# Optimization experiments

Hardware: AMD Instinct MI355X
Metric: run time of the kernel (lower is better)

Reference implementation:

```python
import jax, jax.numpy as jnp
import numpy as np

EMBED = 64
ATT_FACTOR = 10
N_FIELDS = 50
BATCH = 2048


def setup_inputs() -> dict:
    key = jax.random.key(0)
    k_x, k_w, k_h, k_p = jax.random.split(key, 4)
    x = jax.random.normal(k_x, (BATCH, N_FIELDS, EMBED), dtype=jnp.float32)
    # xavier-normal-ish init for params
    attention_W = jax.random.normal(k_w, (EMBED, ATT_FACTOR), dtype=jnp.float32) * (2.0 / (EMBED + ATT_FACTOR)) ** 0.5
    attention_b = jnp.zeros((ATT_FACTOR,), dtype=jnp.float32)
    projection_h = jax.random.normal(k_h, (ATT_FACTOR, 1), dtype=jnp.float32) * (2.0 / (ATT_FACTOR + 1)) ** 0.5
    projection_p = jax.random.normal(k_p, (EMBED, 1), dtype=jnp.float32) * (2.0 / (EMBED + 1)) ** 0.5
    return {"x": x, "attention_W": attention_W, "attention_b": attention_b,
            "projection_h": projection_h, "projection_p": projection_p}


def reference(x, attention_W, attention_b, projection_h, projection_p):
    F_ = x.shape[1]
    idx_i, idx_j = np.triu_indices(F_, k=1)  # all pairs (i<j), P = F*(F-1)/2
    inter = x[:, idx_i, :] * x[:, idx_j, :]  # [B, P, E]
    att_tmp = jax.nn.relu(jnp.einsum('bpe,ef->bpf', inter, attention_W) + attention_b)  # [B,P,A]
    logits = jnp.einsum('bpf,fo->bpo', att_tmp, projection_h)  # [B,P,1]
    score = jax.nn.softmax(logits, axis=1)  # softmax over pairs
    att_out = jnp.sum(score * inter, axis=1)  # [B, E]
    # dropout is identity at inference
    return att_out @ projection_p  # [B, 1]
```

## Files before the change

kernel.cpp:

```cpp
#include <hip/hip_runtime.h>
#include <math.h>


#define F_ 50
#define E_ 64
#define A_ 10
#define XSTR 72
#define NT 256
#define LOG2E 1.44269504088896f

typedef _Float16 half8 __attribute__((ext_vector_type(8)));
typedef _Float16 half4t __attribute__((ext_vector_type(4)));
typedef float f32x4 __attribute__((ext_vector_type(4)));

__global__ __launch_bounds__(NT, 2)
void afm_kernel(const float* __restrict__ x,
                const float* __restrict__ W,
                const float* __restrict__ bias,
                const float* __restrict__ h,
                const float* __restrict__ pp,
                float* __restrict__ out, int nbatch) {
  __shared__ __align__(16) _Float16 sXh[4 * 64 * XSTR];
  __shared__ __align__(16) _Float16 sWh[(A_ + 1) * E_];
  __shared__ float sb[A_], sh[A_];

  const int tid = threadIdx.x;
  const int lane = tid & 63, w4 = tid >> 6;
  const int b = blockIdx.x * 4 + w4;
  const bool bvalid = b < nbatch;
  _Float16* xb = sXh + w4 * (64 * XSTR);

  if (bvalid) {
    const float4* xs = (const float4*)(x + (size_t)b * (F_ * E_));
    for (int q = lane; q < F_ * 16; q += 64) {
      float4 v = xs[q];
      int f = q >> 4, e4 = q & 15;
      half4t hv = {(_Float16)v.x, (_Float16)v.y, (_Float16)v.z, (_Float16)v.w};
      *(half4t*)(xb + f * XSTR + e4 * 4) = hv;
    }
  }
  for (int q = lane; q < 14 * 8; q += 64) {
    int f = F_ + (q >> 3), c = q & 7;
    half8 z = {};
    *(half8*)(xb + f * XSTR + c * 8) = z;
  }
  if (tid < 11 * 16) {
    int k = tid >> 4, e4 = tid & 15;
    float v0, v1, v2, v3;
    if (k < A_) {
      v0 = W[(e4 * 4 + 0) * A_ + k]; v1 = W[(e4 * 4 + 1) * A_ + k];
      v2 = W[(e4 * 4 + 2) * A_ + k]; v3 = W[(e4 * 4 + 3) * A_ + k];
    } else {
      float4 t4 = *(const float4*)(pp + e4 * 4);
      v0 = t4.x; v1 = t4.y; v2 = t4.z; v3 = t4.w;
    }
    half4t hv = {(_Float16)v0, (_Float16)v1, (_Float16)v2, (_Float16)v3};
    *(half4t*)(sWh + k * E_ + e4 * 4) = hv;
  }
  if (tid < A_) { sb[tid] = bias[tid]; sh[tid] = h[tid] * LOG2E; }
  __syncthreads();

  float num = 0.f, den = 0.f;
  if (bvalid) {
    const int m = lane & 15, q8 = lane >> 4;
    half8 fr[4][2];
#pragma unroll
    for (int bi = 0; bi < 4; ++bi)
#pragma unroll
      for (int es = 0; es < 2; ++es)
        fr[bi][es] = *(const half8*)(xb + (bi * 16 + m) * XSTR + es * 32 + q8 * 8);

    float lg[10][4];
#pragma unroll
    for (int t0 = 0; t0 < 10; ++t0)
#pragma unroll
      for (int r = 0; r < 4; ++r) lg[t0][r] = 0.f;

#pragma unroll 1
    for (int k = 0; k < A_; ++k) {
      half8 wv0 = *(const half8*)(sWh + k * E_ + q8 * 8);
      half8 wv1 = *(const half8*)(sWh + k * E_ + 32 + q8 * 8);
      float bk = sb[k];
      f32x4 ci = {bk, bk, bk, bk};
      half8 sa0[4];
#pragma unroll
      for (int bi = 0; bi < 4; ++bi) sa0[bi] = fr[bi][0] * wv0;
      f32x4 t[10];
      {
        int idx = 0;
#pragma unroll
        for (int bi = 0; bi < 4; ++bi)
#pragma unroll
          for (int bj = bi; bj < 4; ++bj)
            t[idx++] = __builtin_amdgcn_mfma_f32_16x16x32_f16(sa0[bi], fr[bj][0], ci, 0, 0, 0);
      }
      half8 sa1[4];
#pragma unroll
      for (int bi = 0; bi < 4; ++bi) sa1[bi] = fr[bi][1] * wv1;
      {
        int idx = 0;
#pragma unroll
        for (int bi = 0; bi < 4; ++bi)
#pragma unroll
          for (int bj = bi; bj < 4; ++bj) {
            t[idx] = __builtin_amdgcn_mfma_f32_16x16x32_f16(sa1[bi], fr[bj][1], t[idx], 0, 0, 0);
            ++idx;
          }
      }
      float hk = sh[k];
#pragma unroll
      for (int idx = 0; idx < 10; ++idx)
#pragma unroll
        for (int r = 0; r < 4; ++r)
          lg[idx][r] = fmaf(fmaxf(t[idx][r], 0.f), hk, lg[idx][r]);
    }

    half8 pv0 = *(const half8*)(sWh + A_ * E_ + q8 * 8);
    half8 pv1 = *(const half8*)(sWh + A_ * E_ + 32 + q8 * 8);
    f32x4 z4 = {0.f, 0.f, 0.f, 0.f};
    int idx = 0;
#pragma unroll
    for (int bi = 0; bi < 4; ++bi) {
      half8 pa0 = fr[bi][0] * pv0;
      half8 pa1 = fr[bi][1] * pv1;
#pragma unroll
      for (int bj = bi; bj < 4; ++bj) {
        f32x4 s4 = __builtin_amdgcn_mfma_f32_16x16x32_f16(pa0, fr[bj][0], z4, 0, 0, 0);
        s4 = __builtin_amdgcn_mfma_f32_16x16x32_f16(pa1, fr[bj][1], s4, 0, 0, 0);
#pragma unroll
        for (int r = 0; r < 4; ++r) {
          int irow = bi * 16 + q8 * 4 + r;
          int jcol = bj * 16 + m;
          bool valid = (irow < jcol) && (jcol < F_);
          float w = valid ? exp2f(lg[idx][r]) : 0.f;
          num = fmaf(w, s4[r], num);
          den += w;
        }
        ++idx;
      }
    }
  }

#pragma unroll
  for (int off = 32; off; off >>= 1) {
    num += __shfl_down(num, off);
    den += __shfl_down(den, off);
  }
  if (lane == 0 && bvalid) out[b] = num / den;
}

extern "C" void kernel_launch(void* const* d_in, const int* in_sizes, int n_in,
                              void* d_out, int out_size, void* d_ws, size_t ws_size,
                              hipStream_t stream) {
  const float* x  = (const float*)d_in[0];
  const float* W  = (const float*)d_in[1];
  const float* bb = (const float*)d_in[2];
  const float* h  = (const float*)d_in[3];
  const float* pp = (const float*)d_in[4];
  float* out = (float*)d_out;
  const int nbatch = in_sizes[0] / (F_ * E_);
  const int nblocks = (nbatch + 3) / 4;
  afm_kernel<<<nblocks, NT, 0, stream>>>(x, W, bb, h, pp, out, nbatch);
}
```

Before: 87.92 us.

## Split each batch's pair-tile work across two wavefronts per sample

Each batch element is now handled by two wavefronts instead of one. The 10 upper-triangular 16x16 tiles are split 5/5 between them via compile-time tile tables, and the partial numerator and denominator are combined through shared memory. Launch bounds rise to 4 blocks per CU, and halving the shared x buffer and the per-thread logit registers is meant to raise occupancy and cut per-wave serial MFMA latency. In exchange, 128 threads cooperate on each x load, a block-wide barrier is added, and each wave loads fragments it may not fully use.

```diff
diff --git a/kernel.cpp b/kernel.cpp
--- a/kernel.cpp
+++ b/kernel.cpp
@@ -13,34 +13,116 @@
 typedef _Float16 half4t __attribute__((ext_vector_type(4)));
 typedef float f32x4 __attribute__((ext_vector_type(4)));
 
-__global__ __launch_bounds__(NT, 2)
+template <int PW>
+__device__ __forceinline__ void compute_half(const _Float16* __restrict__ xb,
+                                             const _Float16* __restrict__ sWh,
+                                             const float* __restrict__ sb,
+                                             const float* __restrict__ sh,
+                                             int lane, float& num, float& den) {
+  constexpr int TI[5] = { PW ? 1 : 0, PW ? 1 : 0, PW ? 2 : 0, PW ? 2 : 0, PW ? 3 : 1 };
+  constexpr int TJ[5] = { PW ? 2 : 0, PW ? 3 : 1, PW ? 2 : 2, PW ? 3 : 3, PW ? 3 : 1 };
+  constexpr bool NEED[4] = { PW == 0, true, PW != 0, PW != 0 };
+
+  const int m = lane & 15, q8 = lane >> 4;
+
+  half8 fr[4][2];
+#pragma unroll
+  for (int bi = 0; bi < 4; ++bi)
+#pragma unroll
+    for (int es = 0; es < 2; ++es)
+      fr[bi][es] = *(const half8*)(xb + (bi * 16 + m) * XSTR + es * 32 + q8 * 8);
+
+  float lg[5][4];
+#pragma unroll
+  for (int tt = 0; tt < 5; ++tt)
+#pragma unroll
+    for (int r = 0; r < 4; ++r) lg[tt][r] = 0.f;
+
+#pragma unroll 1
+  for (int k = 0; k < A_; ++k) {
+    half8 wv0 = *(const half8*)(sWh + k * E_ + q8 * 8);
+    half8 wv1 = *(const half8*)(sWh + k * E_ + 32 + q8 * 8);
+    float bk = sb[k];
+    f32x4 ci = { bk, bk, bk, bk };
+    half8 sa[4];
+#pragma unroll
+    for (int bi = 0; bi < 4; ++bi)
+      if constexpr (true) { if (NEED[bi]) sa[bi] = fr[bi][0] * wv0; }
+    f32x4 t[5];
+#pragma unroll
+    for (int tt = 0; tt < 5; ++tt)
+      t[tt] = __builtin_amdgcn_mfma_f32_16x16x32_f16(sa[TI[tt]], fr[TJ[tt]][0], ci, 0, 0, 0);
+#pragma unroll
+    for (int bi = 0; bi < 4; ++bi)
+      if (NEED[bi]) sa[bi] = fr[bi][1] * wv1;
+#pragma unroll
+    for (int tt = 0; tt < 5; ++tt)
+      t[tt] = __builtin_amdgcn_mfma_f32_16x16x32_f16(sa[TI[tt]], fr[TJ[tt]][1], t[tt], 0, 0, 0);
+    float hk = sh[k];
+#pragma unroll
+    for (int tt = 0; tt < 5; ++tt)
+#pragma unroll
+      for (int r = 0; r < 4; ++r)
+        lg[tt][r] = fmaf(fmaxf(t[tt][r], 0.f), hk, lg[tt][r]);
+  }
+
+  half8 pv0 = *(const half8*)(sWh + A_ * E_ + q8 * 8);
+  half8 pv1 = *(const half8*)(sWh + A_ * E_ + 32 + q8 * 8);
+  half8 pa0[4], pa1[4];
+#pragma unroll
+  for (int bi = 0; bi < 4; ++bi)
+    if (NEED[bi]) { pa0[bi] = fr[bi][0] * pv0; pa1[bi] = fr[bi][1] * pv1; }
+  f32x4 z4 = { 0.f, 0.f, 0.f, 0.f };
+#pragma unroll
+  for (int tt = 0; tt < 5; ++tt) {
+    f32x4 s4 = __builtin_amdgcn_mfma_f32_16x16x32_f16(pa0[TI[tt]], fr[TJ[tt]][0], z4, 0, 0, 0);
+    s4 = __builtin_amdgcn_mfma_f32_16x16x32_f16(pa1[TI[tt]], fr[TJ[tt]][1], s4, 0, 0, 0);
+#pragma unroll
+    for (int r = 0; r < 4; ++r) {
+      int irow = TI[tt] * 16 + q8 * 4 + r;
+      int jcol = TJ[tt] * 16 + m;
+      bool valid = (irow < jcol) && (jcol < F_);
+      float w = valid ? exp2f(lg[tt][r]) : 0.f;
+      num = fmaf(w, s4[r], num);
+      den += w;
+    }
+  }
+}
+
+__global__ __launch_bounds__(NT, 4)
 void afm_kernel(const float* __restrict__ x,
                 const float* __restrict__ W,
                 const float* __restrict__ bias,
                 const float* __restrict__ h,
                 const float* __restrict__ pp,
                 float* __restrict__ out, int nbatch) {
-  __shared__ __align__(16) _Float16 sXh[4 * 64 * XSTR];
+  __shared__ __align__(16) _Float16 sXh[2 * 64 * XSTR];
   __shared__ __align__(16) _Float16 sWh[(A_ + 1) * E_];
   __shared__ float sb[A_], sh[A_];
+  __shared__ float rn[4], rd[4];
 
   const int tid = threadIdx.x;
   const int lane = tid & 63, w4 = tid >> 6;
-  const int b = blockIdx.x * 4 + w4;
+  const int pair = tid >> 7, t128 = tid & 127;
+  const int b = blockIdx.x * 2 + pair;
   const bool bvalid = b < nbatch;
-  _Float16* xb = sXh + w4 * (64 * XSTR);
+  _Float16* xb = sXh + pair * (64 * XSTR);
 
   if (bvalid) {
     const float4* xs = (const float4*)(x + (size_t)b * (F_ * E_));
-    for (int q = lane; q < F_ * 16; q += 64) {
-      float4 v = xs[q];
-      int f = q >> 4, e4 = q & 15;
-      half4t hv = {(_Float16)v.x, (_Float16)v.y, (_Float16)v.z, (_Float16)v.w};
-      *(half4t*)(xb + f * XSTR + e4 * 4) = hv;
+#pragma unroll
+    for (int it = 0; it < 7; ++it) {
+      int q = t128 + it * 128;
+      if (it < 6 || q < F_ * 16) {
+        float4 v = xs[q];
+        int f = q >> 4, e4 = q & 15;
+        half4t hv = { (_Float16)v.x, (_Float16)v.y, (_Float16)v.z, (_Float16)v.w };
+        *(half4t*)(xb + f * XSTR + e4 * 4) = hv;
+      }
     }
   }
-  for (int q = lane; q < 14 * 8; q += 64) {
-    int f = F_ + (q >> 3), c = q & 7;
+  if (t128 < 112) {
+    int f = F_ + (t128 >> 3), c = t128 & 7;
     half8 z = {};
     *(half8*)(xb + f * XSTR + c * 8) = z;
   }
@@ -54,7 +136,7 @@
       float4 t4 = *(const float4*)(pp + e4 * 4);
       v0 = t4.x; v1 = t4.y; v2 = t4.z; v3 = t4.w;
     }
-    half4t hv = {(_Float16)v0, (_Float16)v1, (_Float16)v2, (_Float16)v3};
+    half4t hv = { (_Float16)v0, (_Float16)v1, (_Float16)v2, (_Float16)v3 };
     *(half4t*)(sWh + k * E_ + e4 * 4) = hv;
   }
   if (tid < A_) { sb[tid] = bias[tid]; sh[tid] = h[tid] * LOG2E; }
@@ -62,83 +144,8 @@
 
   float num = 0.f, den = 0.f;
   if (bvalid) {
-    const int m = lane & 15, q8 = lane >> 4;
-    half8 fr[4][2];
-#pragma unroll
-    for (int bi = 0; bi < 4; ++bi)
-#pragma unroll
-      for (int es = 0; es < 2; ++es)
-        fr[bi][es] = *(const half8*)(xb + (bi * 16 + m) * XSTR + es * 32 + q8 * 8);
-
-    float lg[10][4];
-#pragma unroll
-    for (int t0 = 0; t0 < 10; ++t0)
-#pragma unroll
-      for (int r = 0; r < 4; ++r) lg[t0][r] = 0.f;
-
-#pragma unroll 1
-    for (int k = 0; k < A_; ++k) {
-      half8 wv0 = *(const half8*)(sWh + k * E_ + q8 * 8);
-      half8 wv1 = *(const half8*)(sWh + k * E_ + 32 + q8 * 8);
-      float bk = sb[k];
-      f32x4 ci = {bk, bk, bk, bk};
-      half8 sa0[4];
-#pragma unroll
-      for (int bi = 0; bi < 4; ++bi) sa0[bi] = fr[bi][0] * wv0;
-      f32x4 t[10];
-      {
-        int idx = 0;
-#pragma unroll
-        for (int bi = 0; bi < 4; ++bi)
-#pragma unroll
-          for (int bj = bi; bj < 4; ++bj)
-            t[idx++] = __builtin_amdgcn_mfma_f32_16x16x32_f16(sa0[bi], fr[bj][0], ci, 0, 0, 0);
-      }
-      half8 sa1[4];
-#pragma unroll
-      for (int bi = 0; bi < 4; ++bi) sa1[bi] = fr[bi][1] * wv1;
-      {
-        int idx = 0;
-#pragma unroll
-        for (int bi = 0; bi < 4; ++bi)
-#pragma unroll
-          for (int bj = bi; bj < 4; ++bj) {
-            t[idx] = __builtin_amdgcn_mfma_f32_16x16x32_f16(sa1[bi], fr[bj][1], t[idx], 0, 0, 0);
-            ++idx;
-          }
-      }
-      float hk = sh[k];
-#pragma unroll
-      for (int idx = 0; idx < 10; ++idx)
-#pragma unroll
-        for (int r = 0; r < 4; ++r)
-          lg[idx][r] = fmaf(fmaxf(t[idx][r], 0.f), hk, lg[idx][r]);
-    }
-
-    half8 pv0 = *(const half8*)(sWh + A_ * E_ + q8 * 8);
-    half8 pv1 = *(const half8*)(sWh + A_ * E_ + 32 + q8 * 8);
-    f32x4 z4 = {0.f, 0.f, 0.f, 0.f};
-    int idx = 0;
-#pragma unroll
-    for (int bi = 0; bi < 4; ++bi) {
-      half8 pa0 = fr[bi][0] * pv0;
-      half8 pa1 = fr[bi][1] * pv1;
-#pragma unroll
-      for (int bj = bi; bj < 4; ++bj) {
-        f32x4 s4 = __builtin_amdgcn_mfma_f32_16x16x32_f16(pa0, fr[bj][0], z4, 0, 0, 0);
-        s4 = __builtin_amdgcn_mfma_f32_16x16x32_f16(pa1, fr[bj][1], s4, 0, 0, 0);
-#pragma unroll
-        for (int r = 0; r < 4; ++r) {
-          int irow = bi * 16 + q8 * 4 + r;
-          int jcol = bj * 16 + m;
-          bool valid = (irow < jcol) && (jcol < F_);
-          float w = valid ? exp2f(lg[idx][r]) : 0.f;
-          num = fmaf(w, s4[r], num);
-          den += w;
-        }
-        ++idx;
-      }
-    }
+    if ((w4 & 1) == 0) compute_half<0>(xb, sWh, sb, sh, lane, num, den);
+    else               compute_half<1>(xb, sWh, sb, sh, lane, num, den);
   }
 
 #pragma unroll
@@ -146,7 +153,10 @@
     num += __shfl_down(num, off);
     den += __shfl_down(den, off);
   }
-  if (lane == 0 && bvalid) out[b] = num / den;
+  if (lane == 0) { rn[w4] = num; rd[w4] = den; }
+  __syncthreads();
+  if ((tid == 0 || tid == 128) && bvalid)
+    out[b] = (rn[pair * 2] + rn[pair * 2 + 1]) / (rd[pair * 2] + rd[pair * 2 + 1]);
 }
 
 extern "C" void kernel_launch(void* const* d_in, const int* in_sizes, int n_in,
@@ -159,6 +169,6 @@
   const float* pp = (const float*)d_in[4];
   float* out = (float*)d_out;
   const int nbatch = in_sizes[0] / (F_ * E_);
-  const int nblocks = (nbatch + 3) / 4;
+  const int nblocks = (nbatch + 1) / 2;
   afm_kernel<<<nblocks, NT, 0, stream>>>(x, W, bb, h, pp, out, nbatch);
 }
```

After: 86.99 us. No clear change (-1.1%).
